# Kernel tuning notes

Hardware: AMD Instinct MI355X
Metric: run time of the kernel (lower is better)

The kernel has to match this reference:

```python
import jax, jax.numpy as jnp
import numpy as np

DT = 0.5  # integration time step (init_kwargs dt)


def setup_inputs() -> dict:
    key = jax.random.key(0)
    ks = jax.random.split(key, 6)
    B, T, I, H, O = 64, 1024, 64, 512, 64
    g, g_in = 1.0, 1.0
    return {
        "input": jax.random.normal(ks[0], (B, T, I), dtype=jnp.float32),
        "wi": jax.random.normal(ks[1], (I, H), dtype=jnp.float32) * (g_in / np.sqrt(H)),
        "wrec": jax.random.normal(ks[2], (H, H), dtype=jnp.float32) * (g / np.sqrt(H)),
        "wo": jax.random.normal(ks[3], (H, O), dtype=jnp.float32) * (1.0 / np.sqrt(H)),
        "brec": jnp.zeros((H,), dtype=jnp.float32),
        "h0": jax.random.uniform(ks[4], (H,), dtype=jnp.float32, minval=-1.0, maxval=1.0),
    }


def reference(input, wi, wrec, wo, brec, h0):
    # ML_RNN=True, nonlinearity=tanh, readout=id, noise_std=0.0
    B = input.shape[0]
    # Precompute input projection for all timesteps: [B, T, H]
    xproj = jnp.einsum("bti,ih->bth", input, wi) + brec
    h_init = jnp.broadcast_to(h0, (B, h0.shape[0]))

    def step(h, x_t):
        rec = jnp.tanh(h @ wrec.T + x_t)  # [B, H]
        h_new = (1.0 - DT) * h + DT * rec
        return h_new, h_new

    # scan over time: xproj transposed to [T, B, H]
    _, hs = jax.lax.scan(step, h_init, jnp.swapaxes(xproj, 0, 1))
    hs = jnp.swapaxes(hs, 0, 1)  # [B, T, H]
    output = jnp.einsum("bth,ho->bto", hs, wo)  # readout nonlinearity = id
    return output
```

## Files before the change

### kernel.cpp

```cpp
#include <hip/hip_runtime.h>

#define Tn 1024
#define Bn 64
#define In_ 64
#define Hn 512
#define On 64
#define DTC 0.5f

typedef __attribute__((ext_vector_type(8))) short short8;
typedef __attribute__((ext_vector_type(4))) short short4v;
typedef __attribute__((ext_vector_type(4))) float floatx4;
typedef unsigned long long u64;

__device__ __forceinline__ float bf2f(unsigned short u){
  union{unsigned int i; float f;} v; v.i = ((unsigned int)u)<<16; return v.f;
}
__device__ __forceinline__ unsigned short f2bf(float f){
  union{float f; unsigned int i;} v; v.f=f;
  unsigned int x=v.i;
  return (unsigned short)((x + 0x7fffu + ((x>>16)&1u))>>16);
}
__device__ __forceinline__ short8 cvt8(const float* p){
  short8 v;
  #pragma unroll
  for (int e=0;e<8;e++) v[e] = (short)f2bf(p[e]);
  return v;
}
__device__ __forceinline__ void barrier_lds(){
  asm volatile("s_waitcnt lgkmcnt(0)\n\ts_barrier" ::: "memory");
}

__global__ __launch_bounds__(256,2) void xproj_kernel(
    const float* __restrict__ inp, const float* __restrict__ wi,
    const float* __restrict__ brec, unsigned short* __restrict__ xp)
{
  const int t = blockIdx.x, tid = threadIdx.x;
  const int wv = tid>>6, lane = tid&63, col = lane&15, quad = lane>>4;
  __shared__ __align__(16) unsigned short inA[64*80];
  {
    int r = tid>>2, i0 = (tid&3)*16;
    const float* src = inp + ((size_t)r*Tn + t)*In_ + i0;
    unsigned short tmp[16];
    #pragma unroll
    for (int q=0;q<16;q++) tmp[q] = f2bf(src[q]);
    *(short8*)&inA[r*80 + i0]     = *(short8*)&tmp[0];
    *(short8*)&inA[r*80 + i0 + 8] = *(short8*)&tmp[8];
  }
  const int wnb = wv*128;
  short8 bw[8][2];
  float brecv[8];
  #pragma unroll
  for (int nt=0;nt<8;nt++){
    int j = wnb + nt*16 + col;
    brecv[nt] = brec[j];
    #pragma unroll
    for (int ks=0;ks<2;ks++){
      float tmp[8];
      #pragma unroll
      for (int e=0;e<8;e++) tmp[e] = wi[(size_t)(ks*32 + quad*8 + e)*Hn + j];
      bw[nt][ks] = cvt8(tmp);
    }
  }
  __syncthreads();
  floatx4 acc[4][8];
  #pragma unroll
  for (int mt=0;mt<4;mt++)
    #pragma unroll
    for (int nt=0;nt<8;nt++) acc[mt][nt] = (floatx4){0.f,0.f,0.f,0.f};
  #pragma unroll
  for (int ks=0;ks<2;ks++)
    #pragma unroll
    for (int mt=0;mt<4;mt++){
      short8 ar = *(const short8*)&inA[(mt*16+col)*80 + ks*32 + quad*8];
      #pragma unroll
      for (int nt=0;nt<8;nt++)
        acc[mt][nt] = __builtin_amdgcn_mfma_f32_16x16x32_bf16(ar, bw[nt][ks], acc[mt][nt],0,0,0);
    }
  #pragma unroll
  for (int mt=0;mt<4;mt++)
    #pragma unroll
    for (int nt=0;nt<8;nt++)
      #pragma unroll
      for (int r=0;r<4;r++){
        int b = mt*16 + quad*4 + r;
        int j = wnb + nt*16 + col;
        xp[((size_t)t*Bn + b)*Hn + j] = f2bf(acc[mt][nt][r] + brecv[nt]);
      }
}

__global__ __launch_bounds__(256,1) void wrec_pack(
    const float* __restrict__ wrec, unsigned short* __restrict__ wrecB)
{
  int gl = blockIdx.x*256 + threadIdx.x;
  int fi = gl>>6, lane = gl&63;
  int gmt = fi>>1, ksx = fi&1;
  int j = gmt*16 + (lane&15);
  int k = 320 + ksx*32 + (lane>>4)*8;
  short8 v = cvt8(wrec + (size_t)j*Hn + k);
  *(short8*)(wrecB + (size_t)gl*8) = v;
}

__global__ __launch_bounds__(512,2) void rnn_scan(
    const float* __restrict__ wrec, const float* __restrict__ h0,
    const unsigned short* xp,
    const unsigned short* __restrict__ wrecB,
    unsigned short* hs)
{
  const int tid  = threadIdx.x;
  const int g    = blockIdx.x;
  const int wv   = tid >> 6;
  const int lane = tid & 63;
  const int col  = lane & 15;
  const int quad = lane >> 4;
  const int wbase = wv*64;

  __shared__ __align__(16) unsigned short wrecL[65536];
  __shared__ __align__(16) unsigned short hA[8192];

  short8 awr[4][10];
  #pragma unroll
  for (int mt=0;mt<4;mt++)
    #pragma unroll
    for (int ks=0;ks<10;ks++){
      int j = wbase + mt*16 + col;
      int k = ks*32 + quad*8;
      awr[mt][ks] = cvt8(wrec + (size_t)j*Hn + k);
    }
  #pragma unroll
  for (int mt=0;mt<4;mt++)
    #pragma unroll
    for (int ks2=0;ks2<4;ks2++){
      int j = wbase + mt*16 + col;
      int k = 384 + ks2*32 + quad*8;
      short8 v = cvt8(wrec + (size_t)j*Hn + k);
      *(short8*)&wrecL[(((wv*4+mt)*4 + ks2))*512 + lane*8] = v;
    }
  for (int idx = tid; idx < 16*Hn; idx += 512){
    int b = idx >> 9, k = idx & 511;
    hA[(((k>>5)*64 + ((k>>3)&3)*16 + b))*8 + (k&7)] = f2bf(h0[k]);
  }
  float hm[4][4];
  #pragma unroll
  for (int mt=0;mt<4;mt++)
    #pragma unroll
    for (int r=0;r<4;r++) hm[mt][r] = h0[wbase + mt*16 + quad*4 + r];

  floatx4 acc[4];
  #pragma unroll
  for (int mt=0;mt<4;mt++) acc[mt] = (floatx4){0.f,0.f,0.f,0.f};

  const size_t row = (size_t)(g*16 + col);
  __syncthreads();

  for (int t = 0; t < Tn; t++){
    short8 wst[4];
    u64 xv[4];
    #pragma unroll
    for (int mt=0;mt<4;mt++)
      wst[mt] = *(const short8*)(wrecB + (size_t)(((wv*4+mt)*2 + 0)*64 + lane)*8);
    #pragma unroll
    for (int mt=0;mt<4;mt++)
      xv[mt] = *(const u64*)(xp + (size_t)t*(Bn*Hn) + row*Hn + wbase + mt*16 + quad*4);

    #pragma unroll
    for (int ks=0;ks<10;ks++){
      short8 hb = *(const short8*)&hA[ks*512 + lane*8];
      #pragma unroll
      for (int mt=0;mt<4;mt++)
        acc[mt] = __builtin_amdgcn_mfma_f32_16x16x32_bf16(awr[mt][ks], hb, acc[mt],0,0,0);
    }
    {
      short8 hb = *(const short8*)&hA[10*512 + lane*8];
      #pragma unroll
      for (int mt=0;mt<4;mt++)
        acc[mt] = __builtin_amdgcn_mfma_f32_16x16x32_bf16(wst[mt], hb, acc[mt],0,0,0);
    }
    #pragma unroll
    for (int mt=0;mt<4;mt++)
      wst[mt] = *(const short8*)(wrecB + (size_t)(((wv*4+mt)*2 + 1)*64 + lane)*8);
    #pragma unroll
    for (int ks2=0;ks2<4;ks2++){
      short8 hb = *(const short8*)&hA[(12+ks2)*512 + lane*8];
      #pragma unroll
      for (int mt=0;mt<4;mt++){
        short8 aw = *(const short8*)&wrecL[(((wv*4+mt)*4 + ks2))*512 + lane*8];
        acc[mt] = __builtin_amdgcn_mfma_f32_16x16x32_bf16(aw, hb, acc[mt],0,0,0);
      }
    }
    {
      short8 hb = *(const short8*)&hA[11*512 + lane*8];
      #pragma unroll
      for (int mt=0;mt<4;mt++)
        acc[mt] = __builtin_amdgcn_mfma_f32_16x16x32_bf16(wst[mt], hb, acc[mt],0,0,0);
    }

    barrier_lds();

    #pragma unroll
    for (int mt=0;mt<4;mt++){
      u64 x = xv[mt];
      unsigned short hv[4];
      #pragma unroll
      for (int r=0;r<4;r++){
        float pre = acc[mt][r] + bf2f((unsigned short)(x >> (16*r)));
        float e2x = __expf(2.0f*pre);
        float rec = 1.0f - 2.0f/(e2x + 1.0f);
        float hn  = (1.0f-DTC)*hm[mt][r] + DTC*rec;
        hm[mt][r] = hn;
        hv[r] = f2bf(hn);
      }
      int j4 = wbase + mt*16 + quad*4;
      *(short4v*)&hA[(((j4>>5)*64 + ((j4>>3)&3)*16 + col))*8 + (j4&7)] = *(short4v*)hv;
      u64 pk = (u64)hv[0] | ((u64)hv[1]<<16) | ((u64)hv[2]<<32) | ((u64)hv[3]<<48);
      __builtin_nontemporal_store(pk, (u64*)(hs + (size_t)t*(Bn*Hn) + row*Hn + j4));
      acc[mt] = (floatx4){0.f,0.f,0.f,0.f};
    }
    barrier_lds();
  }
}

__global__ __launch_bounds__(256,1) void out_gemm(
    const unsigned short* __restrict__ hs,
    const float* __restrict__ wo,
    float* __restrict__ out)
{
  const int tid = threadIdx.x, bid = blockIdx.x;
  const int wv = tid >> 6, lane = tid & 63, col = lane & 15, quad = lane >> 4;
  const int m0 = bid*64;
  __shared__ __align__(16) unsigned short hsA[64][520];

  for (int c = tid; c < 64*64; c += 256){
    int r = c >> 6, cc = (c & 63)*8;
    *(short8*)&hsA[r][cc] = *(const short8*)(hs + (size_t)(m0 + r)*Hn + cc);
  }
  short8 boh[16], bol[16];
  #pragma unroll
  for (int kk = 0; kk < 16; kk++){
    float tmp[8];
    #pragma unroll
    for (int e = 0; e < 8; e++) tmp[e] = wo[(size_t)(kk*32 + quad*8 + e)*On + wv*16 + col];
    #pragma unroll
    for (int e = 0; e < 8; e++){
      unsigned short h = f2bf(tmp[e]);
      boh[kk][e] = (short)h;
      bol[kk][e] = (short)f2bf(tmp[e] - bf2f(h));
    }
  }
  __syncthreads();

  floatx4 acc[4];
  #pragma unroll
  for (int ms=0;ms<4;ms++) acc[ms] = (floatx4){0.f,0.f,0.f,0.f};
  #pragma unroll
  for (int kk = 0; kk < 16; kk++){
    int k = kk*32 + quad*8;
    #pragma unroll
    for (int ms = 0; ms < 4; ms++){
      short8 a = *(const short8*)&hsA[ms*16 + col][k];
      acc[ms] = __builtin_amdgcn_mfma_f32_16x16x32_bf16(a, boh[kk], acc[ms], 0,0,0);
      acc[ms] = __builtin_amdgcn_mfma_f32_16x16x32_bf16(a, bol[kk], acc[ms], 0,0,0);
    }
  }
  #pragma unroll
  for (int ms = 0; ms < 4; ms++)
    #pragma unroll
    for (int r = 0; r < 4; r++){
      int m = m0 + ms*16 + quad*4 + r;
      int b = m & 63, tt = m >> 6;
      out[((size_t)b*Tn + tt)*On + wv*16 + col] = acc[ms][r];
    }
}

extern "C" void kernel_launch(void* const* d_in, const int* in_sizes, int n_in,
                              void* d_out, int out_size, void* d_ws, size_t ws_size,
                              hipStream_t stream){
  const float* inp  = (const float*)d_in[0];
  const float* wi   = (const float*)d_in[1];
  const float* wrec = (const float*)d_in[2];
  const float* wo   = (const float*)d_in[3];
  const float* brec = (const float*)d_in[4];
  const float* h0   = (const float*)d_in[5];
  float* out = (float*)d_out;

  char* ws = (char*)d_ws;
  unsigned short* hs = (unsigned short*)ws;
  unsigned short* xp = (unsigned short*)(ws + 65536);
  unsigned short* wrecB = (unsigned short*)(ws + (size_t)Tn*Bn*Hn*2 + 65536);

  xproj_kernel<<<Tn, 256, 0, stream>>>(inp, wi, brec, xp);
  wrec_pack  <<<16, 256, 0, stream>>>(wrec, wrecB);
  rnn_scan   <<<4, 512, 0, stream>>>(wrec, h0, xp, wrecB, hs);
  out_gemm   <<<(Bn*Tn)/64, 256, 0, stream>>>(hs, wo, out);
}
```

Measured before the change: 3.492 ms.

## Keep 12 of 16 recurrent-weight K-slices in registers and prepack all of W_rec

The pack kernel now converts the whole recurrent weight matrix to bf16 in MFMA fragment order. The scan kernel keeps 48 fragments per lane in registers, loaded through an inline-asm global load, and places the last 4 K-slices in LDS. This removes the per-timestep global reloads of the two streamed K-slices, and pointer increments replace the per-step address arithmetic. The cost is much higher register pressure (48 short8 fragments per lane at 512 threads), which risks spills or lower occupancy, plus a larger pack launch.

```diff
diff --git a/kernel.cpp b/kernel.cpp
--- a/kernel.cpp
+++ b/kernel.cpp
@@ -28,6 +28,12 @@
 }
 __device__ __forceinline__ void barrier_lds(){
   asm volatile("s_waitcnt lgkmcnt(0)\n\ts_barrier" ::: "memory");
+}
+__device__ __forceinline__ short8 gload16(const unsigned short* p){
+  short8 r;
+  asm volatile("global_load_dwordx4 %0, %1, off\n\ts_waitcnt vmcnt(0)"
+               : "=&v"(r) : "v"(p) : "memory");
+  return r;
 }
 
 __global__ __launch_bounds__(256,2) void xproj_kernel(
@@ -89,21 +95,21 @@
 }
 
 __global__ __launch_bounds__(256,1) void wrec_pack(
-    const float* __restrict__ wrec, unsigned short* __restrict__ wrecB)
+    const float* __restrict__ wrec, unsigned short* __restrict__ wrecP)
 {
   int gl = blockIdx.x*256 + threadIdx.x;
-  int fi = gl>>6, lane = gl&63;
-  int gmt = fi>>1, ksx = fi&1;
-  int j = gmt*16 + (lane&15);
-  int k = 320 + ksx*32 + (lane>>4)*8;
+  int frag = gl>>6, lane = gl&63;
+  int wvmt = frag>>4, ks = frag&15;
+  int j = (wvmt>>2)*64 + (wvmt&3)*16 + (lane&15);
+  int k = ks*32 + (lane>>4)*8;
   short8 v = cvt8(wrec + (size_t)j*Hn + k);
-  *(short8*)(wrecB + (size_t)gl*8) = v;
+  *(short8*)(wrecP + (size_t)gl*8) = v;
 }
 
 __global__ __launch_bounds__(512,2) void rnn_scan(
-    const float* __restrict__ wrec, const float* __restrict__ h0,
+    const float* __restrict__ h0,
     const unsigned short* xp,
-    const unsigned short* __restrict__ wrecB,
+    const unsigned short* __restrict__ wrecP,
     unsigned short* hs)
 {
   const int tid  = threadIdx.x;
@@ -117,24 +123,20 @@
   __shared__ __align__(16) unsigned short wrecL[65536];
   __shared__ __align__(16) unsigned short hA[8192];
 
-  short8 awr[4][10];
-  #pragma unroll
-  for (int mt=0;mt<4;mt++)
-    #pragma unroll
-    for (int ks=0;ks<10;ks++){
-      int j = wbase + mt*16 + col;
-      int k = ks*32 + quad*8;
-      awr[mt][ks] = cvt8(wrec + (size_t)j*Hn + k);
-    }
-  #pragma unroll
-  for (int mt=0;mt<4;mt++)
-    #pragma unroll
-    for (int ks2=0;ks2<4;ks2++){
-      int j = wbase + mt*16 + col;
-      int k = 384 + ks2*32 + quad*8;
-      short8 v = cvt8(wrec + (size_t)j*Hn + k);
-      *(short8*)&wrecL[(((wv*4+mt)*4 + ks2))*512 + lane*8] = v;
-    }
+  short8 awr[48];
+  #pragma unroll
+  for (int mt=0;mt<4;mt++)
+    #pragma unroll
+    for (int ks=0;ks<12;ks++)
+      awr[mt*12+ks] = gload16(wrecP + (size_t)(((wv*4+mt)*16 + ks)*64 + lane)*8);
+
+  #pragma unroll
+  for (int mt=0;mt<4;mt++)
+    #pragma unroll
+    for (int ks2=0;ks2<4;ks2++)
+      *(short8*)&wrecL[(((wv*4+mt)*4 + ks2))*512 + lane*8] =
+        *(const short8*)(wrecP + (size_t)(((wv*4+mt)*16 + 12 + ks2)*64 + lane)*8);
+
   for (int idx = tid; idx < 16*Hn; idx += 512){
     int b = idx >> 9, k = idx & 511;
     hA[(((k>>5)*64 + ((k>>3)&3)*16 + b))*8 + (k&7)] = f2bf(h0[k]);
@@ -150,34 +152,23 @@
   for (int mt=0;mt<4;mt++) acc[mt] = (floatx4){0.f,0.f,0.f,0.f};
 
   const size_t row = (size_t)(g*16 + col);
+  const unsigned short* xpp = xp + row*Hn + wbase;
+  unsigned short* hsp = hs + row*Hn + wbase;
   __syncthreads();
 
   for (int t = 0; t < Tn; t++){
-    short8 wst[4];
     u64 xv[4];
     #pragma unroll
     for (int mt=0;mt<4;mt++)
-      wst[mt] = *(const short8*)(wrecB + (size_t)(((wv*4+mt)*2 + 0)*64 + lane)*8);
-    #pragma unroll
-    for (int mt=0;mt<4;mt++)
-      xv[mt] = *(const u64*)(xp + (size_t)t*(Bn*Hn) + row*Hn + wbase + mt*16 + quad*4);
-
-    #pragma unroll
-    for (int ks=0;ks<10;ks++){
+      xv[mt] = *(const u64*)(xpp + mt*16 + quad*4);
+
+    #pragma unroll
+    for (int ks=0;ks<12;ks++){
       short8 hb = *(const short8*)&hA[ks*512 + lane*8];
       #pragma unroll
       for (int mt=0;mt<4;mt++)
-        acc[mt] = __builtin_amdgcn_mfma_f32_16x16x32_bf16(awr[mt][ks], hb, acc[mt],0,0,0);
-    }
-    {
-      short8 hb = *(const short8*)&hA[10*512 + lane*8];
-      #pragma unroll
-      for (int mt=0;mt<4;mt++)
-        acc[mt] = __builtin_amdgcn_mfma_f32_16x16x32_bf16(wst[mt], hb, acc[mt],0,0,0);
-    }
-    #pragma unroll
-    for (int mt=0;mt<4;mt++)
-      wst[mt] = *(const short8*)(wrecB + (size_t)(((wv*4+mt)*2 + 1)*64 + lane)*8);
+        acc[mt] = __builtin_amdgcn_mfma_f32_16x16x32_bf16(awr[mt*12+ks], hb, acc[mt],0,0,0);
+    }
     #pragma unroll
     for (int ks2=0;ks2<4;ks2++){
       short8 hb = *(const short8*)&hA[(12+ks2)*512 + lane*8];
@@ -186,12 +177,6 @@
         short8 aw = *(const short8*)&wrecL[(((wv*4+mt)*4 + ks2))*512 + lane*8];
         acc[mt] = __builtin_amdgcn_mfma_f32_16x16x32_bf16(aw, hb, acc[mt],0,0,0);
       }
-    }
-    {
-      short8 hb = *(const short8*)&hA[11*512 + lane*8];
-      #pragma unroll
-      for (int mt=0;mt<4;mt++)
-        acc[mt] = __builtin_amdgcn_mfma_f32_16x16x32_bf16(wst[mt], hb, acc[mt],0,0,0);
     }
 
     barrier_lds();
@@ -212,9 +197,11 @@
       int j4 = wbase + mt*16 + quad*4;
       *(short4v*)&hA[(((j4>>5)*64 + ((j4>>3)&3)*16 + col))*8 + (j4&7)] = *(short4v*)hv;
       u64 pk = (u64)hv[0] | ((u64)hv[1]<<16) | ((u64)hv[2]<<32) | ((u64)hv[3]<<48);
-      __builtin_nontemporal_store(pk, (u64*)(hs + (size_t)t*(Bn*Hn) + row*Hn + j4));
+      __builtin_nontemporal_store(pk, (u64*)(hsp + mt*16 + quad*4));
       acc[mt] = (floatx4){0.f,0.f,0.f,0.f};
     }
+    xpp += Bn*Hn;
+    hsp += Bn*Hn;
     barrier_lds();
   }
 }
@@ -285,10 +272,10 @@
   char* ws = (char*)d_ws;
   unsigned short* hs = (unsigned short*)ws;
   unsigned short* xp = (unsigned short*)(ws + 65536);
-  unsigned short* wrecB = (unsigned short*)(ws + (size_t)Tn*Bn*Hn*2 + 65536);
+  unsigned short* wrecP = (unsigned short*)(ws + (size_t)Tn*Bn*Hn*2 + 65536);
 
   xproj_kernel<<<Tn, 256, 0, stream>>>(inp, wi, brec, xp);
-  wrec_pack  <<<16, 256, 0, stream>>>(wrec, wrecB);
-  rnn_scan   <<<4, 512, 0, stream>>>(wrec, h0, xp, wrecB, hs);
+  wrec_pack  <<<128, 256, 0, stream>>>(wrec, wrecP);
+  rnn_scan   <<<4, 512, 0, stream>>>(h0, xp, wrecP, hs);
   out_gemm   <<<(Bn*Tn)/64, 256, 0, stream>>>(hs, wo, out);
 }
```

Measured after the change: 4.469 ms. 1.28x slower.
